# Performance work log

Measured on AMD Instinct MI355X. Metric: run time of the kernel, lower is better.

Reference implementation:

```python
import jax, jax.numpy as jnp
import numpy as np

N_WIRES = 8
DIM = 2 ** N_WIRES  # 256 amplitudes
# PauliZ sign table: Z_SIGNS[w, i] = +1 if bit w of basis index i is 0 else -1
_bits = (np.arange(DIM)[None, :] >> (N_WIRES - 1 - np.arange(N_WIRES))[:, None]) & 1
Z_SIGNS = jnp.asarray(1.0 - 2.0 * _bits, dtype=jnp.float32)  # [8, 256]


def quantum_project(t, theta):
    """Batched 8-wire circuit: RX(x_w) encoder + trainable RX(theta_w) (RX gates on the
    same wire compose additively), then CNOT ring, then <Z_w> for each wire.
    t: [B, S, E] -> returns [B, S, H, 8]."""
    B, S, E = t.shape
    H = E // N_WIRES
    ang = (t.reshape(B, S, H, N_WIRES) + theta) * 0.5  # RX(a)RX(b)=RX(a+b)
    q0 = jnp.cos(ang).astype(jnp.complex64)
    q1 = (-1j * jnp.sin(ang)).astype(jnp.complex64)
    # Build product state |psi> = \otimes_w [cos(a_w/2), -i sin(a_w/2)] -> [B,S,H,256]
    state = jnp.ones((B, S, H, 1), jnp.complex64)
    for w in range(N_WIRES):
        qb = jnp.stack([q0[..., w], q1[..., w]], axis=-1)  # [B,S,H,2]
        state = (state[..., :, None] * qb[..., None, :]).reshape(B, S, H, -1)
    state = state.reshape((B, S, H) + (2,) * N_WIRES)  # wire w on axis 3+w
    # CNOT chain 0->1,...,6->7 then ring-closing 7->0
    for cw, tw in [(w, w + 1) for w in range(N_WIRES - 1)] + [(N_WIRES - 1, 0)]:
        s0 = jax.lax.index_in_dim(state, 0, axis=3 + cw, keepdims=True)
        s1 = jnp.flip(jax.lax.index_in_dim(state, 1, axis=3 + cw, keepdims=True), axis=3 + tw)
        state = jnp.concatenate([s0, s1], axis=3 + cw)
    amps = state.reshape(B, S, H, DIM)
    probs = amps.real * amps.real + amps.imag * amps.imag  # [B,S,H,256] float32
    return jnp.einsum('bshd,wd->bshw', probs, Z_SIGNS)  # <Z_w> per wire


def setup_inputs() -> dict:
    key = jax.random.key(0)
    kx, kq, kk, kv, ko, kt = jax.random.split(key, 6)
    B, S, E = 16, 512, 64
    scale = 1.0 / np.sqrt(E)
    return {
        'x': jax.random.normal(kx, (B, S, E), dtype=jnp.float32),
        'Wq': jax.random.normal(kq, (E, E), dtype=jnp.float32) * scale,
        'Wk': jax.random.normal(kk, (E, E), dtype=jnp.float32) * scale,
        'Wv': jax.random.normal(kv, (E, E), dtype=jnp.float32) * scale,
        'Wo': jax.random.normal(ko, (E, E), dtype=jnp.float32) * scale,
        'theta': jax.random.uniform(kt, (N_WIRES,), dtype=jnp.float32, minval=0.0, maxval=2.0 * np.pi),
    }


def reference(x, Wq, Wk, Wv, Wo, theta):
    B, S, E = x.shape
    q = quantum_project(x @ Wq.T, theta)  # [B,S,H,8]
    k = quantum_project(x @ Wk.T, theta)
    v = quantum_project(x @ Wv.T, theta)
    # NOTE: original code never transposes heads to dim 1, so attention mixes HEADS
    # per token: scores [B,S,H,H]. Faithfully reproduced. d_k = 8.
    scores = jnp.einsum('bsiw,bsjw->bsij', q, k) / jnp.float32(np.sqrt(N_WIRES))
    attn = jax.nn.softmax(scores, axis=-1)  # dropout is identity in eval
    out = jnp.einsum('bsij,bsjw->bsiw', attn, v)  # [B,S,H,8]
    # original: out.transpose(1,2).contiguous().view(B,-1,E) -> scrambled layout
    out = out.transpose(0, 2, 1, 3).reshape(B, -1, E)
    return out @ Wo.T
```

## Files before the change

kernel.cpp:

```cpp
#include <hip/hip_runtime.h>


typedef float  f32x4  __attribute__((ext_vector_type(4)));
typedef short  bf16x8 __attribute__((ext_vector_type(8)));
typedef unsigned short u16;
typedef unsigned int   u32;

#define WRS 72
#define SPS 68

#define DPP_SHR_STEP(d, j, sh)                                                 \
    {                                                                          \
        float _t = __int_as_float(__builtin_amdgcn_update_dpp(                 \
            0x3f800000, __float_as_int(d), 0x110 + sh, 0xf, 0xf, false));      \
        d *= ((j) >= (sh)) ? _t : 1.0f;                                        \
    }

__device__ __forceinline__ u32 bfh(float f) {
    const u32 u = __float_as_uint(f);
    return (u + 0x7FFFu + ((u >> 16) & 1u)) >> 16;
}
__device__ __forceinline__ void bfsplit2(float a, float b, u32& h, u32& l) {
    const u32 ua = __float_as_uint(a), ub = __float_as_uint(b);
    h = (ua >> 16) | (ub & 0xFFFF0000u);
    const float ra = a - __uint_as_float(ua & 0xFFFF0000u);
    const float rb = b - __uint_as_float(ub & 0xFFFF0000u);
    l = bfh(ra) | (bfh(rb) << 16);
}
__device__ __forceinline__ bf16x8 mk8(u32 a, u32 b, u32 c, u32 d) {
    uint4 t = make_uint4(a, b, c, d);
    return *(bf16x8*)&t;
}
__device__ __forceinline__ void splitpack(const float4 w0, const float4 w1,
                                          bf16x8& hi, bf16x8& lo) {
    u32 h0, l0, h1, l1, h2, l2, h3, l3;
    bfsplit2(w0.x, w0.y, h0, l0);
    bfsplit2(w0.z, w0.w, h1, l1);
    bfsplit2(w1.x, w1.y, h2, l2);
    bfsplit2(w1.z, w1.w, h3, l3);
    hi = mk8(h0, h1, h2, h3);
    lo = mk8(l0, l1, l2, l3);
}

#define MFMA3(acc, ah, al, bh, bl)                                             \
    acc = __builtin_amdgcn_mfma_f32_16x16x32_bf16(al, bh, acc, 0, 0, 0);       \
    acc = __builtin_amdgcn_mfma_f32_16x16x32_bf16(ah, bl, acc, 0, 0, 0);       \
    acc = __builtin_amdgcn_mfma_f32_16x16x32_bf16(ah, bh, acc, 0, 0, 0);

__global__ __launch_bounds__(256, 4)
void qattn_fused(const float* __restrict__ xg,
                 const float* __restrict__ wqg, const float* __restrict__ wkg,
                 const float* __restrict__ wvg, const float* __restrict__ wog,
                 const float* __restrict__ thg,
                 float* __restrict__ outg)
{
    __shared__ u16 sXh[16 * WRS];
    __shared__ u16 sXl[16 * WRS];
    __shared__ __align__(16) float sP[48 * SPS];
    __shared__ u16 sSh[16 * WRS];
    __shared__ u16 sSl[16 * WRS];

    const int tid  = threadIdx.x;
    const int lane = tid & 63;
    const int wg   = tid >> 6;
    const int l15  = lane & 15;
    const int quad = lane >> 4;
    const int j    = lane & 7;
    const int b    = blockIdx.x >> 5;
    const int grp  = blockIdx.x & 31;

    {
        const float4 v = ((const float4*)(xg + (size_t)(b * 512 + grp * 16) * 64))[tid];
        u32 h01, l01, h23, l23;
        bfsplit2(v.x, v.y, h01, l01);
        bfsplit2(v.z, v.w, h23, l23);
        const int o = (tid >> 4) * WRS + 4 * (tid & 15);
        *(uint2*)&sXh[o] = make_uint2(h01, h23);
        *(uint2*)&sXl[o] = make_uint2(l01, l23);
    }
    const float thf = thg[j];
    __syncthreads();

    {
        const int arow = l15 * WRS + quad * 8;
        const bf16x8 ah0 = *(const bf16x8*)&sXh[arow];
        const bf16x8 ah1 = *(const bf16x8*)&sXh[arow + 32];
        const bf16x8 al0 = *(const bf16x8*)&sXl[arow];
        const bf16x8 al1 = *(const bf16x8*)&sXl[arow + 32];
        #pragma unroll
        for (int ia = 0; ia < 3; ++ia) {
            const int aid = wg * 3 + ia;
            const int m = aid >> 2, nt = aid & 3;
            const float* wm = (m == 0) ? wqg : (m == 1) ? wkg : wvg;
            const float* wr = wm + (nt * 16 + l15) * 64 + quad * 8;
            bf16x8 bh0, bl0, bh1, bl1;
            {
                const float4 w0 = *(const float4*)wr;
                const float4 w1 = *(const float4*)(wr + 4);
                splitpack(w0, w1, bh0, bl0);
            }
            {
                const float4 w0 = *(const float4*)(wr + 32);
                const float4 w1 = *(const float4*)(wr + 36);
                splitpack(w0, w1, bh1, bl1);
            }
            f32x4 acc = {0.f, 0.f, 0.f, 0.f};
            MFMA3(acc, ah0, al0, bh0, bl0)
            MFMA3(acc, ah1, al1, bh1, bl1)
            #pragma unroll
            for (int r = 0; r < 4; ++r) {
                const float c = __cosf(acc[r] + thf);
                float d = c;
                DPP_SHR_STEP(d, j, 1)
                DPP_SHR_STEP(d, j, 2)
                DPP_SHR_STEP(d, j, 4)
                float ex = (j == 0) ? 1.0f : c;
                DPP_SHR_STEP(ex, j, 1)
                DPP_SHR_STEP(ex, j, 2)
                DPP_SHR_STEP(ex, j, 4)
                const int row  = m * 16 + quad * 4 + r;
                const int base = row * SPS + nt * 16 + l15;
                if (j > 0)  sP[base]     = d;
                if (j == 7) sP[base - 7] = ex;
            }
        }
    }
    __syncthreads();

    {
        const int tg = wg * 4 + (lane >> 4);
        const int i  = j;
        const int qb = tg * SPS;
        const int kb = (16 + tg) * SPS;
        const int vb = (32 + tg) * SPS;
        float q[8];
        *(float4*)&q[0] = *(const float4*)&sP[qb + 8 * i];
        *(float4*)&q[4] = *(const float4*)&sP[qb + 8 * i + 4];
        float pr[8];
        float sum = 0.f;
        #pragma unroll
        for (int jj = 0; jj < 8; ++jj) {
            const float4 k0 = *(const float4*)&sP[kb + 8 * jj];
            const float4 k1 = *(const float4*)&sP[kb + 8 * jj + 4];
            float s = q[0] * k0.x;
            s = fmaf(q[1], k0.y, s); s = fmaf(q[2], k0.z, s);
            s = fmaf(q[3], k0.w, s); s = fmaf(q[4], k1.x, s);
            s = fmaf(q[5], k1.y, s); s = fmaf(q[6], k1.z, s);
            s = fmaf(q[7], k1.w, s);
            pr[jj] = __expf(s * 0.35355339059327373f);
            sum += pr[jj];
        }
        const float rinv = 1.0f / sum;
        float o[8];
        #pragma unroll
        for (int w = 0; w < 8; ++w) o[w] = 0.f;
        #pragma unroll
        for (int jj = 0; jj < 8; ++jj) {
            const float4 v0 = *(const float4*)&sP[vb + 8 * jj];
            const float4 v1 = *(const float4*)&sP[vb + 8 * jj + 4];
            const float a = pr[jj] * rinv;
            o[0] = fmaf(a, v0.x, o[0]); o[1] = fmaf(a, v0.y, o[1]);
            o[2] = fmaf(a, v0.z, o[2]); o[3] = fmaf(a, v0.w, o[3]);
            o[4] = fmaf(a, v1.x, o[4]); o[5] = fmaf(a, v1.y, o[5]);
            o[6] = fmaf(a, v1.z, o[6]); o[7] = fmaf(a, v1.w, o[7]);
        }
        if (!(lane & 8)) {
            u32 hh[4], ll[4];
            #pragma unroll
            for (int c = 0; c < 4; ++c)
                bfsplit2(o[2 * c], o[2 * c + 1], hh[c], ll[c]);
            const int so = (i * 2 + (tg >> 3)) * WRS + 8 * (tg & 7);
            *(uint4*)&sSh[so] = make_uint4(hh[0], hh[1], hh[2], hh[3]);
            *(uint4*)&sSl[so] = make_uint4(ll[0], ll[1], ll[2], ll[3]);
        }
    }
    __syncthreads();

    {
        const int arow = l15 * WRS + quad * 8;
        const bf16x8 ah0 = *(const bf16x8*)&sSh[arow];
        const bf16x8 ah1 = *(const bf16x8*)&sSh[arow + 32];
        const bf16x8 al0 = *(const bf16x8*)&sSl[arow];
        const bf16x8 al1 = *(const bf16x8*)&sSl[arow + 32];
        const float* wr = wog + (wg * 16 + l15) * 64 + quad * 8;
        bf16x8 bh0, bl0, bh1, bl1;
        {
            const float4 w0 = *(const float4*)wr;
            const float4 w1 = *(const float4*)(wr + 4);
            splitpack(w0, w1, bh0, bl0);
        }
        {
            const float4 w0 = *(const float4*)(wr + 32);
            const float4 w1 = *(const float4*)(wr + 36);
            splitpack(w0, w1, bh1, bl1);
        }
        f32x4 acc = {0.f, 0.f, 0.f, 0.f};
        MFMA3(acc, ah0, al0, bh0, bl0)
        MFMA3(acc, ah1, al1, bh1, bl1)
        const int e = wg * 16 + l15;
        #pragma unroll
        for (int r = 0; r < 4; ++r) {
            const int rho = quad * 4 + r;
            const int R   = (rho >> 1) * 64 + grp * 2 + (rho & 1);
            outg[((size_t)(b * 512 + R)) * 64 + e] = acc[r];
        }
    }
}

extern "C" void kernel_launch(void* const* d_in, const int* in_sizes, int n_in,
                              void* d_out, int out_size, void* d_ws, size_t ws_size,
                              hipStream_t stream) {
    const float* x  = (const float*)d_in[0];
    const float* wq = (const float*)d_in[1];
    const float* wk = (const float*)d_in[2];
    const float* wv = (const float*)d_in[3];
    const float* wo = (const float*)d_in[4];
    const float* th = (const float*)d_in[5];
    float* out = (float*)d_out;
    qattn_fused<<<dim3(512), dim3(256), 0, stream>>>(x, wq, wk, wv, wo, th, out);
}
```

Before: 68.37 us.

## Pre-split weights to bf16 hi/lo in a prep kernel; load X directly to registers

Adds a small prep kernel that converts all four weight matrices into bf16 hi/lo halves in workspace, so each of the 512 main blocks loads packed bf16 instead of re-splitting the fp32 weights. The X tile is now read from global memory straight into MFMA operand registers, which removes its LDS staging and one __syncthreads. The cost is an extra kernel launch plus a workspace round trip, and each wavefront now loads X redundantly from global memory rather than sharing it through LDS.

```diff
diff --git a/kernel.cpp b/kernel.cpp
--- a/kernel.cpp
+++ b/kernel.cpp
@@ -47,15 +47,27 @@
     acc = __builtin_amdgcn_mfma_f32_16x16x32_bf16(ah, bl, acc, 0, 0, 0);       \
     acc = __builtin_amdgcn_mfma_f32_16x16x32_bf16(ah, bh, acc, 0, 0, 0);
 
+__global__ __launch_bounds__(256)
+void prep_w(const float* __restrict__ wq, const float* __restrict__ wk,
+            const float* __restrict__ wv, const float* __restrict__ wo,
+            u16* __restrict__ whi, u16* __restrict__ wlo)
+{
+    const int g = blockIdx.x * 256 + threadIdx.x;
+    const float* gm[4] = {wq, wk, wv, wo};
+    const float4 v = ((const float4*)gm[g >> 10])[g & 1023];
+    u32 h01, l01, h23, l23;
+    bfsplit2(v.x, v.y, h01, l01);
+    bfsplit2(v.z, v.w, h23, l23);
+    *(uint2*)&whi[4 * g] = make_uint2(h01, h23);
+    *(uint2*)&wlo[4 * g] = make_uint2(l01, l23);
+}
+
 __global__ __launch_bounds__(256, 4)
 void qattn_fused(const float* __restrict__ xg,
-                 const float* __restrict__ wqg, const float* __restrict__ wkg,
-                 const float* __restrict__ wvg, const float* __restrict__ wog,
+                 const u16* __restrict__ whi, const u16* __restrict__ wlo,
                  const float* __restrict__ thg,
                  float* __restrict__ outg)
 {
-    __shared__ u16 sXh[16 * WRS];
-    __shared__ u16 sXl[16 * WRS];
     __shared__ __align__(16) float sP[48 * SPS];
     __shared__ u16 sSh[16 * WRS];
     __shared__ u16 sSl[16 * WRS];
@@ -69,41 +81,30 @@
     const int b    = blockIdx.x >> 5;
     const int grp  = blockIdx.x & 31;
 
+    const float thf = thg[j];
+
     {
-        const float4 v = ((const float4*)(xg + (size_t)(b * 512 + grp * 16) * 64))[tid];
-        u32 h01, l01, h23, l23;
-        bfsplit2(v.x, v.y, h01, l01);
-        bfsplit2(v.z, v.w, h23, l23);
-        const int o = (tid >> 4) * WRS + 4 * (tid & 15);
-        *(uint2*)&sXh[o] = make_uint2(h01, h23);
-        *(uint2*)&sXl[o] = make_uint2(l01, l23);
-    }
-    const float thf = thg[j];
-    __syncthreads();
-
-    {
-        const int arow = l15 * WRS + quad * 8;
-        const bf16x8 ah0 = *(const bf16x8*)&sXh[arow];
-        const bf16x8 ah1 = *(const bf16x8*)&sXh[arow + 32];
-        const bf16x8 al0 = *(const bf16x8*)&sXl[arow];
-        const bf16x8 al1 = *(const bf16x8*)&sXl[arow + 32];
+        const float* xr = xg + (size_t)(b * 512 + grp * 16 + l15) * 64 + quad * 8;
+        bf16x8 ah0, al0, ah1, al1;
+        {
+            const float4 x0 = *(const float4*)xr;
+            const float4 x1 = *(const float4*)(xr + 4);
+            splitpack(x0, x1, ah0, al0);
+        }
+        {
+            const float4 x0 = *(const float4*)(xr + 32);
+            const float4 x1 = *(const float4*)(xr + 36);
+            splitpack(x0, x1, ah1, al1);
+        }
         #pragma unroll
         for (int ia = 0; ia < 3; ++ia) {
             const int aid = wg * 3 + ia;
             const int m = aid >> 2, nt = aid & 3;
-            const float* wm = (m == 0) ? wqg : (m == 1) ? wkg : wvg;
-            const float* wr = wm + (nt * 16 + l15) * 64 + quad * 8;
-            bf16x8 bh0, bl0, bh1, bl1;
-            {
-                const float4 w0 = *(const float4*)wr;
-                const float4 w1 = *(const float4*)(wr + 4);
-                splitpack(w0, w1, bh0, bl0);
-            }
-            {
-                const float4 w0 = *(const float4*)(wr + 32);
-                const float4 w1 = *(const float4*)(wr + 36);
-                splitpack(w0, w1, bh1, bl1);
-            }
+            const int off = ((m * 64 + nt * 16 + l15) * 64) + quad * 8;
+            const bf16x8 bh0 = *(const bf16x8*)(whi + off);
+            const bf16x8 bh1 = *(const bf16x8*)(whi + off + 32);
+            const bf16x8 bl0 = *(const bf16x8*)(wlo + off);
+            const bf16x8 bl1 = *(const bf16x8*)(wlo + off + 32);
             f32x4 acc = {0.f, 0.f, 0.f, 0.f};
             MFMA3(acc, ah0, al0, bh0, bl0)
             MFMA3(acc, ah1, al1, bh1, bl1)
@@ -182,18 +183,11 @@
         const bf16x8 ah1 = *(const bf16x8*)&sSh[arow + 32];
         const bf16x8 al0 = *(const bf16x8*)&sSl[arow];
         const bf16x8 al1 = *(const bf16x8*)&sSl[arow + 32];
-        const float* wr = wog + (wg * 16 + l15) * 64 + quad * 8;
-        bf16x8 bh0, bl0, bh1, bl1;
-        {
-            const float4 w0 = *(const float4*)wr;
-            const float4 w1 = *(const float4*)(wr + 4);
-            splitpack(w0, w1, bh0, bl0);
-        }
-        {
-            const float4 w0 = *(const float4*)(wr + 32);
-            const float4 w1 = *(const float4*)(wr + 36);
-            splitpack(w0, w1, bh1, bl1);
-        }
+        const int off = ((3 * 64 + wg * 16 + l15) * 64) + quad * 8;
+        const bf16x8 bh0 = *(const bf16x8*)(whi + off);
+        const bf16x8 bh1 = *(const bf16x8*)(whi + off + 32);
+        const bf16x8 bl0 = *(const bf16x8*)(wlo + off);
+        const bf16x8 bl1 = *(const bf16x8*)(wlo + off + 32);
         f32x4 acc = {0.f, 0.f, 0.f, 0.f};
         MFMA3(acc, ah0, al0, bh0, bl0)
         MFMA3(acc, ah1, al1, bh1, bl1)
@@ -217,5 +211,8 @@
     const float* wo = (const float*)d_in[4];
     const float* th = (const float*)d_in[5];
     float* out = (float*)d_out;
-    qattn_fused<<<dim3(512), dim3(256), 0, stream>>>(x, wq, wk, wv, wo, th, out);
-}
+    u16* whi = (u16*)d_ws;
+    u16* wlo = whi + 4 * 64 * 64;
+    prep_w<<<dim3(16), dim3(256), 0, stream>>>(wq, wk, wv, wo, whi, wlo);
+    qattn_fused<<<dim3(512), dim3(256), 0, stream>>>(x, whi, wlo, th, out);
+}
```

Result: slower. 70.56 us (+3.2%).
